# Optimization experiments

Hardware: AMD Instinct MI355X
Metric: run time of the kernel (lower is better)

## Reference

```python
import jax, jax.numpy as jnp
import numpy as np

EPS = 1e-5
INF = 1e5


def setup_inputs() -> dict:
    key = jax.random.key(0)
    ks = iter(jax.random.split(key, 32))
    B, N, F, H, NH, C = 2, 384, 64, 64, 4, 32
    def lin(k, fi, fo):
        return jax.random.normal(k, (fi, fo), jnp.float32) / np.sqrt(fi).astype(np.float32)
    d = {}
    d['h'] = jax.random.normal(next(ks), (B, N, F), jnp.float32)
    d['x'] = jax.random.normal(next(ks), (B, N, 3), jnp.float32)
    # edge_model (ConcatenationFilter): Linear(2F+1,H), SiLU, Linear(H,H), SiLU
    d['We0'] = lin(next(ks), 2 * F + 1, H); d['be0'] = jnp.zeros(H, jnp.float32)
    d['We1'] = lin(next(ks), H, H);         d['be1'] = jnp.zeros(H, jnp.float32)
    # semantic_attention_mlp: Linear(H, n_heads), LeakyReLU(0.2)
    d['Ws'] = lin(next(ks), H, NH);         d['bs'] = jnp.zeros(NH, jnp.float32)
    # coefficients_mlp: Linear(H,H), SiLU, Linear(H,C)
    d['Wc0'] = lin(next(ks), H, H);         d['bc0'] = jnp.zeros(H, jnp.float32)
    d['Wc1'] = lin(next(ks), H, C);         d['bc1'] = jnp.zeros(C, jnp.float32)
    # post_norm_mlp: Linear(C,H), SiLU, Linear(H,H)
    d['Wp0'] = lin(next(ks), C, H);         d['bp0'] = jnp.zeros(H, jnp.float32)
    d['Wp1'] = lin(next(ks), H, H);         d['bp1'] = jnp.zeros(H, jnp.float32)
    # coordinate_mlp: Linear(H,H), SiLU, Linear(H,1,bias=False) init gain 1e-3
    d['Wx0'] = lin(next(ks), H, H);         d['bx0'] = jnp.zeros(H, jnp.float32)
    d['Wx1'] = lin(next(ks), H, 1) * 1e-3
    # node_mlp: Linear(NH*H + H + F, H), SiLU, Linear(H, F)
    d['Wn0'] = lin(next(ks), NH * H + H + F, H); d['bn0'] = jnp.zeros(H, jnp.float32)
    d['Wn1'] = lin(next(ks), H, F);         d['bn1'] = jnp.zeros(F, jnp.float32)
    d['log_gamma'] = jnp.zeros(NH, jnp.float32)
    return d


def _forward(h, x, We0, be0, We1, be1, Ws, bs, Wc0, bc0, Wc1, bc1,
             Wp0, bp0, Wp1, bp1, Wx0, bx0, Wx1, Wn0, bn0, Wn1, bn1, log_gamma):
    B, N, F = h.shape
    silu = jax.nn.silu

    # pairwise displacements and distances: (B,N,N,3), (B,N,N,1)
    x_minus_xt = x[:, :, None, :] - x[:, None, :, :]
    norm = jnp.sqrt(jnp.sum(x_minus_xt * x_minus_xt, axis=-1, keepdims=True) + EPS)

    # pairwise node-feature concat + distance -> edge MLP (ConcatenationFilter)
    hi = jnp.broadcast_to(h[:, :, None, :], (B, N, N, F))
    hj = jnp.broadcast_to(h[:, None, :, :], (B, N, N, F))
    e_in = jnp.concatenate([hi, hj, norm], axis=-1)           # (B,N,N,2F+1)
    h_e = silu(silu(e_in @ We0 + be0) @ We1 + be1)            # (B,N,N,H)

    eye = jnp.eye(N, dtype=h.dtype)[None, :, :, None]         # mask self-edges

    # euclidean attention per head, softmax over neighbors j (axis=-2)
    eu = jax.nn.softmax(-(norm + INF * eye) * jnp.exp(log_gamma), axis=-2)  # (B,N,N,NH)
    # semantic attention
    sem_logits = jax.nn.leaky_relu(h_e @ Ws + bs, 0.2) - INF * eye
    sem = jax.nn.softmax(sem_logits, axis=-2)                 # (B,N,N,NH)
    comb = eu * sem
    comb = comb / (jnp.sum(comb, axis=-2, keepdims=True) + EPS)

    # attention-weighted multi-head edge features, aggregated over neighbors
    h_e_att = (comb[..., :, None] * h_e[..., None, :]).reshape(B, N, N, -1)  # (B,N,N,NH*H)
    h_e_agg = jnp.sum(h_e_att, axis=-2)                       # (B,N,NH*H)

    # spatial attention: equivariant combinations of unit direction vectors
    coeff = silu(h_e @ Wc0 + bc0) @ Wc1 + bc1                 # (B,N,N,C)
    x_hat = x_minus_xt / (norm + EPS)                         # (B,N,N,3)
    combinations = coeff[..., :, None] * x_hat[..., None, :]  # (B,N,N,C,3)
    comb_sum = jnp.mean(combinations, axis=2)                 # mean over j -> (B,N,C,3)
    comb_norm = jnp.sum(comb_sum * comb_sum, axis=-1)         # (B,N,C)
    h_comb = silu(comb_norm @ Wp0 + bp0) @ Wp1 + bp1          # (B,N,H)

    # node update (residual)
    node_in = jnp.concatenate([h, h_e_agg, h_comb], axis=-1)
    h_out = h + (silu(node_in @ Wn0 + bn0) @ Wn1 + bn1)

    # coordinate update: scalar-gated displacements, mean over neighbors
    scale = silu(h_e @ Wx0 + bx0) @ Wx1                       # (B,N,N,1)
    x_out = x + jnp.mean(x_minus_xt * scale, axis=2)          # (B,N,3)
    return h_out, x_out


def reference(h, x, We0, be0, We1, be1, Ws, bs, Wc0, bc0, Wc1, bc1,
              Wp0, bp0, Wp1, bp1, Wx0, bx0, Wx1, Wn0, bn0, Wn1, bn1, log_gamma):
    return _forward(h, x, We0, be0, We1, be1, Ws, bs, Wc0, bc0, Wc1, bc1,
                    Wp0, bp0, Wp1, bp1, Wx0, bx0, Wx1, Wn0, bn0, Wn1, bn1, log_gamma)
```

## Files before the change

kernel.cpp:

```cpp
#include <hip/hip_runtime.h>

#define NPT 384
#define NB 2
#define NROW (NB*NPT)
#define NT 6
#define HOFF 49152
#define RECB 1024
#define REC_OFF 424960

typedef unsigned short u16;
typedef unsigned int u32;
typedef __bf16 bf16x8 __attribute__((ext_vector_type(8)));
typedef float f32x4 __attribute__((ext_vector_type(4)));

struct alignas(16) U4 { u32 x, y, z, w; };
struct alignas(8)  U2 { u32 x, y; };

constexpr float kEPS = 1e-5f;
constexpr float kINF = 1e5f;

__device__ __forceinline__ u16 f2b(float f) { __bf16 b = (__bf16)f; return __builtin_bit_cast(u16, b); }
__device__ __forceinline__ u32 pk2(float lo, float hi) { return (u32)f2b(lo) | ((u32)f2b(hi) << 16); }
__device__ __forceinline__ float b2f(u32 u) { return __uint_as_float(u << 16); }
__device__ __forceinline__ float silu_f(float v) { return v * __builtin_amdgcn_rcpf(1.f + __expf(-v)); }
__device__ __forceinline__ float wredmax(float v) {
#pragma unroll
  for (int m = 32; m >= 1; m >>= 1) v = fmaxf(v, __shfl_xor(v, m, 64));
  return v;
}
__device__ __forceinline__ float wredsum(float v) {
#pragma unroll
  for (int m = 32; m >= 1; m >>= 1) v += __shfl_xor(v, m, 64);
  return v;
}
__device__ __forceinline__ void up8(U4 u, float* f) {
  f[0] = b2f(u.x & 0xffffu); f[1] = b2f(u.x >> 16);
  f[2] = b2f(u.y & 0xffffu); f[3] = b2f(u.y >> 16);
  f[4] = b2f(u.z & 0xffffu); f[5] = b2f(u.z >> 16);
  f[6] = b2f(u.w & 0xffffu); f[7] = b2f(u.w >> 16);
}

__global__ __launch_bounds__(64) void sake_prep(
    const float* __restrict__ h, const float* __restrict__ We0,
    const float* __restrict__ be0, const float* __restrict__ We1,
    const float* __restrict__ Wc0, const float* __restrict__ Wc1,
    const float* __restrict__ Wx0, const float* __restrict__ Ws,
    float* __restrict__ U, float* __restrict__ V, u16* __restrict__ WT)
{
  const int t = threadIdx.x;
  const int blk = blockIdx.x;
  if (blk < NROW) {
    __shared__ float hs[64];
    hs[t] = h[blk * 64 + t];
    __syncthreads();
    float u = be0[t], v = 0.f;
#pragma unroll 8
    for (int k = 0; k < 64; k++) {
      float hv = hs[k];
      u = fmaf(hv, We0[k * 64 + t], u);
      v = fmaf(hv, We0[(64 + k) * 64 + t], v);
    }
    U[blk * 64 + t] = u;
    V[blk * 64 + t] = v;
  } else {
    const int wsel = blk - NROW;
    if (wsel == 4) {
      u16* dst = WT + 14336;
      for (int o = t; o < 16 * 64; o += 64) {
        int c = o >> 6, k = o & 63;
        dst[o] = (c < 4) ? f2b(Ws[k * 4 + c]) : (u16)0;
      }
      return;
    }
    const float* src; int nout; u16* dst;
    if      (wsel == 0) { src = We1; nout = 64; dst = WT;         }
    else if (wsel == 1) { src = Wc0; nout = 64; dst = WT + 4096;  }
    else if (wsel == 2) { src = Wx0; nout = 64; dst = WT + 8192;  }
    else                { src = Wc1; nout = 32; dst = WT + 12288; }
    const int total = 64 * nout;
    for (int o = t; o < total; o += 64) {
      int n = o >> 6, k = o & 63;
      dst[o] = f2b(src[k * nout + n]);
    }
  }
}

struct MainArgs {
  const float *x, *U, *V;
  const u16 *We1T, *Wc0T, *Wx0T, *Wc1T, *WsPT;
  const float *We0, *bs, *be1, *bc0, *bc1, *bx0, *Wx1, *log_gamma;
  char* rec;
};

__device__ __forceinline__ void readB(const u16* tile, int j, int kg, bf16x8& f0, bf16x8& f1) {
  const int r7 = j & 7;
  f0 = *(const bf16x8*)(tile + j * 64 + ((kg ^ r7) << 3));
  f1 = *(const bf16x8*)(tile + j * 64 + (((kg + 4) ^ r7) << 3));
}

template<int NNT, bool SILU_, int NCH, bool DUALT>
__device__ __forceinline__ void gemmT(const u16* __restrict__ wG, const float* __restrict__ biasG,
                                      bf16x8 bf0, bf16x8 bf1, u16* out, u16* oTT, int w, int lane)
{
  const int j = (w << 4) + (lane & 15);
  const int kg = lane >> 4;
  const int jm = j & (NCH - 1);
#pragma unroll
  for (int nt = 0; nt < NNT; nt++) {
    const int nrow = (nt << 4) + (lane & 15);
    bf16x8 a0 = *(const bf16x8*)(wG + nrow * 64 + (kg << 3));
    bf16x8 a1 = *(const bf16x8*)(wG + nrow * 64 + 32 + (kg << 3));
    f32x4 acc = {0.f, 0.f, 0.f, 0.f};
    acc = __builtin_amdgcn_mfma_f32_16x16x32_bf16(a0, bf0, acc, 0, 0, 0);
    acc = __builtin_amdgcn_mfma_f32_16x16x32_bf16(a1, bf1, acc, 0, 0, 0);
    const int n0 = (nt << 4) + (kg << 2);
    const float4 bv = *(const float4*)(biasG + n0);
    float s0, s1, s2, s3;
    if constexpr (SILU_) {
      s0 = silu_f(acc[0] + bv.x); s1 = silu_f(acc[1] + bv.y);
      s2 = silu_f(acc[2] + bv.z); s3 = silu_f(acc[3] + bv.w);
    } else {
      s0 = acc[0] + bv.x; s1 = acc[1] + bv.y;
      s2 = acc[2] + bv.z; s3 = acc[3] + bv.w;
    }
    const u16 q0 = f2b(s0), q1 = f2b(s1), q2 = f2b(s2), q3 = f2b(s3);
    U2 pkd; pkd.x = (u32)q0 | ((u32)q1 << 16); pkd.y = (u32)q2 | ((u32)q3 << 16);
    const int c = n0 >> 3;
    *(U2*)(out + j * (NCH * 8) + (((c ^ jm) << 3) + (n0 & 7))) = pkd;
    if constexpr (DUALT) {
      const int jq = (j >> 3), j7 = j & 7;
      const u16 qs[4] = {q0, q1, q2, q3};
#pragma unroll
      for (int r = 0; r < 4; r++) {
        const int f = n0 + r;
        oTT[f * 64 + ((jq ^ (f & 7)) << 3) + j7] = qs[r];
      }
    }
  }
}

__global__ __launch_bounds__(256, 4) void sake_main(MainArgs A)
{
  __shared__ __align__(16) u16 buf0[64 * 64];
  __shared__ __align__(16) u16 hes[64 * 64];
  __shared__ __align__(16) u16 hesT[64 * 64];
  __shared__ __align__(16) u16 coeff[64 * 32];
  __shared__ __align__(16) u16 E_lds[16 * 64];
  __shared__ float raw_lds[64 * 5];
  __shared__ float disp[64][3];
  __shared__ float nrm_s[64];

  const int t = threadIdx.x;
  const int w = t >> 6, lane = t & 63;
  const int bt = blockIdx.x;
  const int i = bt % NPT;
  const int bj = bt / NPT;
  const int jt = bj % NT, b = bj / NT;
  const int bi = b * NPT + i;
  const int j0 = jt << 6;
  const int jj2 = t >> 2, q4 = t & 3;
  char* rec = A.rec + (size_t)(bi * NT + jt) * RECB;

  const int jrow = j0 + jj2;
  const float* xp = &A.x[(b * NPT + jrow) * 3];
  const float xj0 = xp[0], xj1 = xp[1], xj2 = xp[2];
  const float xi0 = A.x[bi * 3 + 0], xi1 = A.x[bi * 3 + 1], xi2 = A.x[bi * 3 + 2];
  const float4* vp = (const float4*)(A.V + (size_t)(b * NPT + jrow) * 64 + q4 * 16);
  const float4 v0_ = vp[0], v1_ = vp[1], v2_ = vp[2], v3_ = vp[3];
  const float4* Up = (const float4*)(A.U + bi * 64 + q4 * 16);
  const float4 u0_ = Up[0], u1_ = Up[1], u2_ = Up[2], u3_ = Up[3];
  const float4* Wd = (const float4*)(A.We0 + 128 * 64 + q4 * 16);
  const float4 w0_ = Wd[0], w1_ = Wd[1], w2_ = Wd[2], w3_ = Wd[3];

  {
    float dx0 = xi0 - xj0, dx1 = xi1 - xj1, dx2 = xi2 - xj2;
    float nr = sqrtf(fmaf(dx0, dx0, fmaf(dx1, dx1, fmaf(dx2, dx2, kEPS))));
    if (q4 == 0) { disp[jj2][0] = dx0; disp[jj2][1] = dx1; disp[jj2][2] = dx2; nrm_s[jj2] = nr; }
    float vv[16] = {v0_.x, v0_.y, v0_.z, v0_.w, v1_.x, v1_.y, v1_.z, v1_.w,
                    v2_.x, v2_.y, v2_.z, v2_.w, v3_.x, v3_.y, v3_.z, v3_.w};
    float uu[16] = {u0_.x, u0_.y, u0_.z, u0_.w, u1_.x, u1_.y, u1_.z, u1_.w,
                    u2_.x, u2_.y, u2_.z, u2_.w, u3_.x, u3_.y, u3_.z, u3_.w};
    float ww[16] = {w0_.x, w0_.y, w0_.z, w0_.w, w1_.x, w1_.y, w1_.z, w1_.w,
                    w2_.x, w2_.y, w2_.z, w2_.w, w3_.x, w3_.y, w3_.z, w3_.w};
    float sv[16];
#pragma unroll
    for (int e = 0; e < 16; e++) sv[e] = silu_f(uu[e] + vv[e] + nr * ww[e]);
    U4 lo, hi;
    lo.x = pk2(sv[0], sv[1]);   lo.y = pk2(sv[2], sv[3]);
    lo.z = pk2(sv[4], sv[5]);   lo.w = pk2(sv[6], sv[7]);
    hi.x = pk2(sv[8], sv[9]);   hi.y = pk2(sv[10], sv[11]);
    hi.z = pk2(sv[12], sv[13]); hi.w = pk2(sv[14], sv[15]);
    const int r7 = jj2 & 7;
    *(U4*)(buf0 + jj2 * 64 + (((q4 * 2) ^ r7) << 3)) = lo;
    *(U4*)(buf0 + jj2 * 64 + (((q4 * 2 + 1) ^ r7) << 3)) = hi;
  }

  const int j = (w << 4) + (lane & 15);
  const int kg = lane >> 4;

  bf16x8 bh0, bh1;
  readB(buf0, j, kg, bh0, bh1);
  gemmT<4, true, 8, true>(A.We1T, A.be1, bh0, bh1, hes, hesT, w, lane);

  bf16x8 he0, he1;
  readB(hes, j, kg, he0, he1);

  gemmT<4, true, 8, false>(A.Wc0T, A.bc0, he0, he1, buf0, nullptr, w, lane);
  bf16x8 c10, c11;
  readB(buf0, j, kg, c10, c11);
  gemmT<2, false, 4, false>(A.Wc1T, A.bc1, c10, c11, coeff, nullptr, w, lane);

  float cA0 = 0, cA1 = 0, cA2 = 0, xA0 = 0, xA1 = 0, xA2 = 0;
  {
    const int c = t & 31, g = t >> 5;
    const int cc = c >> 3, ce = c & 7;
#pragma unroll
    for (int it = 0; it < 8; ++it) {
      const int jj = (g << 3) + it;
      const float s = b2f(coeff[jj * 32 + ((cc ^ (jj & 3)) << 3) + ce]) *
                      __builtin_amdgcn_rcpf(nrm_s[jj] + kEPS);
      cA0 = fmaf(s, disp[jj][0], cA0);
      cA1 = fmaf(s, disp[jj][1], cA1);
      cA2 = fmaf(s, disp[jj][2], cA2);
    }
  }

  gemmT<4, true, 8, false>(A.Wx0T, A.bx0, he0, he1, buf0, nullptr, w, lane);

  {
    const int jj = jj2;
    const int r7 = jj & 7;
    float acc = 0.f;
#pragma unroll
    for (int c2 = 0; c2 < 2; c2++) {
      const int c = q4 * 2 + c2;
      U4 u = *(const U4*)(buf0 + jj * 64 + ((c ^ r7) << 3));
      float f8[8]; up8(u, f8);
      const float4* wx = (const float4*)(A.Wx1 + c * 8);
      const float4 wxa = wx[0], wxb = wx[1];
      acc = fmaf(f8[0], wxa.x, acc); acc = fmaf(f8[1], wxa.y, acc);
      acc = fmaf(f8[2], wxa.z, acc); acc = fmaf(f8[3], wxa.w, acc);
      acc = fmaf(f8[4], wxb.x, acc); acc = fmaf(f8[5], wxb.y, acc);
      acc = fmaf(f8[6], wxb.z, acc); acc = fmaf(f8[7], wxb.w, acc);
    }
    acc += __shfl_xor(acc, 1, 64);
    acc += __shfl_xor(acc, 2, 64);
    if (q4 == 0) {
      xA0 = fmaf(disp[jj][0], acc, xA0);
      xA1 = fmaf(disp[jj][1], acc, xA1);
      xA2 = fmaf(disp[jj][2], acc, xA2);
    }
  }

  {
    const int m0 = w << 4;
    const int arow = m0 + (lane & 15);
    const int r7a = arow & 7;
    bf16x8 a0 = *(const bf16x8*)(hes + arow * 64 + ((kg ^ r7a) << 3));
    bf16x8 a1 = *(const bf16x8*)(hes + arow * 64 + (((kg + 4) ^ r7a) << 3));
    const u16* wrow = A.WsPT + (lane & 15) * 64;
    bf16x8 b0 = *(const bf16x8*)(wrow + (kg << 3));
    bf16x8 b1 = *(const bf16x8*)(wrow + 32 + (kg << 3));
    f32x4 acc = {0.f, 0.f, 0.f, 0.f};
    acc = __builtin_amdgcn_mfma_f32_16x16x32_bf16(a0, b0, acc, 0, 0, 0);
    acc = __builtin_amdgcn_mfma_f32_16x16x32_bf16(a1, b1, acc, 0, 0, 0);
    if ((lane & 15) < 4) {
#pragma unroll
      for (int r = 0; r < 4; r++)
        raw_lds[(m0 + (kg << 2) + r) * 5 + (lane & 15)] = acc[r];
    }
  }
  __syncthreads();

  float* cascr = (float*)buf0;
  float* xscr = (float*)buf0 + 768;
  cascr[t * 3 + 0] = cA0; cascr[t * 3 + 1] = cA1; cascr[t * 3 + 2] = cA2;
  if (q4 == 0) { xscr[jj2 * 3 + 0] = xA0; xscr[jj2 * 3 + 1] = xA1; xscr[jj2 * 3 + 2] = xA2; }

  {
    const int jj = lane, head = w;
    float raw = raw_lds[jj * 5 + head] + A.bs[head];
    float bsem = (raw > 0.f) ? raw : 0.2f * raw;
    const bool self = (j0 + jj) == i;
    if (self) bsem -= kINF;
    const float gam = __expf(A.log_gamma[head]);
    const float aeu = -(nrm_s[jj] + (self ? kINF : 0.f)) * gam;
    const float L = aeu + bsem;
    const float mL = wredmax(L);
    const float eL = __expf(L - mL);
    const float SL = wredsum(eL);
    const float mb = wredmax(bsem);
    const float Sb = wredsum(__expf(bsem - mb));
    const float Sa = wredsum(__expf(aeu));
    E_lds[head * 64 + (((jj >> 3) ^ head) << 3) + (jj & 7)] = f2b(eL);
    if (lane == 0) {
      float* sp = (float*)(rec + 908) + head * 5;
      sp[0] = mL; sp[1] = SL; sp[2] = mb; sp[3] = Sb; sp[4] = Sa;
    }
  }
  __syncthreads();

  {
    const int erow = lane & 15;
    const int e7 = erow & 7;
    bf16x8 ea0 = *(const bf16x8*)(E_lds + erow * 64 + ((kg ^ e7) << 3));
    bf16x8 ea1 = *(const bf16x8*)(E_lds + erow * 64 + (((kg + 4) ^ e7) << 3));
    const int f = (w << 4) + (lane & 15);
    const int f7 = f & 7;
    bf16x8 hb0 = *(const bf16x8*)(hesT + f * 64 + ((kg ^ f7) << 3));
    bf16x8 hb1 = *(const bf16x8*)(hesT + f * 64 + (((kg + 4) ^ f7) << 3));
    f32x4 aF = {0.f, 0.f, 0.f, 0.f};
    aF = __builtin_amdgcn_mfma_f32_16x16x32_bf16(ea0, hb0, aF, 0, 0, 0);
    aF = __builtin_amdgcn_mfma_f32_16x16x32_bf16(ea1, hb1, aF, 0, 0, 0);
    if (kg == 0) {
      u16* rA = (u16*)rec;
#pragma unroll
      for (int r = 0; r < 4; r++) rA[r * 64 + f] = f2b(aF[r]);
    }
  }
  if (t < 96) {
    const int c = t & 31, d = t >> 5;
    float s = 0.f;
#pragma unroll
    for (int g = 0; g < 8; g++) s += cascr[(g * 32 + c) * 3 + d];
    ((float*)(rec + 512))[d * 32 + c] = s;
  } else if (t < 99) {
    const int d = t - 96;
    float s = 0.f;
    for (int k = 0; k < 64; k++) s += xscr[k * 3 + d];
    ((float*)(rec + 896))[d] = s;
  }
}

struct MergeArgs {
  const float *h, *x, *Wp0, *bp0, *Wp1, *bp1, *Wn0, *bn0, *Wn1, *bn1;
  const char* rec;
  float* out;
};

__global__ __launch_bounds__(256) void sake_merge(MergeArgs M)
{
  __shared__ float sc[NT][20];
  __shared__ float wAl[NT][4];
  __shared__ float coefh[4];
  __shared__ float node_in[384];
  __shared__ float cmv[96];
  __shared__ float nrm32[32];
  __shared__ float t0s[64];
  __shared__ float scr[256];

  const int t = threadIdx.x;
  const int bi = blockIdx.x;
  const char* rb = M.rec + (size_t)bi * NT * RECB;

  if (t < NT * 20) {
    const int tt = t / 20, k = t % 20;
    sc[tt][k] = ((const float*)(rb + tt * RECB + 908))[k];
  }
  if (t < 64) node_in[t] = M.h[bi * 64 + t];
  __syncthreads();
  if (t < 4) {
    const int hh = t;
    float mL = -1e30f, mb = -1e30f;
    for (int tt = 0; tt < NT; tt++) {
      mL = fmaxf(mL, sc[tt][hh * 5 + 0]);
      mb = fmaxf(mb, sc[tt][hh * 5 + 2]);
    }
    float SL = 0.f, Sb = 0.f, Sa = 0.f;
    for (int tt = 0; tt < NT; tt++) {
      const float wa = __expf(sc[tt][hh * 5 + 0] - mL);
      wAl[tt][hh] = wa;
      SL = fmaf(wa, sc[tt][hh * 5 + 1], SL);
      Sb = fmaf(__expf(sc[tt][hh * 5 + 2] - mb), sc[tt][hh * 5 + 3], Sb);
      Sa += sc[tt][hh * 5 + 4];
    }
    const float Ff = __expf(mL - mb);
    coefh[hh] = Ff / fmaf(SL, Ff, kEPS * Sa * Sb);
  }
  __syncthreads();
  {
    const int hh = t >> 6, f = t & 63;
    float s = 0.f;
#pragma unroll
    for (int tt = 0; tt < NT; tt++)
      s = fmaf(wAl[tt][hh], b2f(((const u16*)(rb + tt * RECB))[hh * 64 + f]), s);
    node_in[64 + hh * 64 + f] = s * coefh[hh];
  }
  if (t < 96) {
    float s = 0.f;
#pragma unroll
    for (int tt = 0; tt < NT; tt++) s += ((const float*)(rb + tt * RECB + 512))[t];
    cmv[t] = s * (1.f / 384.f);
  }
  if (t >= 128 && t < 131) {
    const int d = t - 128;
    float s = 0.f;
#pragma unroll
    for (int tt = 0; tt < NT; tt++) s += ((const float*)(rb + tt * RECB + 896))[d];
    M.out[HOFF + bi * 3 + d] = M.x[bi * 3 + d] + s * (1.f / 384.f);
  }
  __syncthreads();
  if (t < 32) {
    const float v0 = cmv[t], v1 = cmv[32 + t], v2 = cmv[64 + t];
    nrm32[t] = v0 * v0 + v1 * v1 + v2 * v2;
  }
  __syncthreads();
  if (t < 64) {
    float a = M.bp0[t];
    for (int c = 0; c < 32; c++) a = fmaf(nrm32[c], M.Wp0[c * 64 + t], a);
    t0s[t] = silu_f(a);
  }
  __syncthreads();
  if (t < 64) {
    float a = M.bp1[t];
    for (int k = 0; k < 64; k++) a = fmaf(t0s[k], M.Wp1[k * 64 + t], a);
    node_in[320 + t] = a;
  }
  __syncthreads();
  {
    const int f = t & 63, q = t >> 6;
    float a = 0.f;
    const int k0 = q * 96;
    for (int k = 0; k < 96; k++) a = fmaf(node_in[k0 + k], M.Wn0[(k0 + k) * 64 + f], a);
    scr[t] = a;
  }
  __syncthreads();
  if (t < 64) {
    const float s = scr[t] + scr[64 + t] + scr[128 + t] + scr[192 + t] + M.bn0[t];
    t0s[t] = silu_f(s);
  }
  __syncthreads();
  if (t < 64) {
    float a = M.bn1[t];
    for (int k = 0; k < 64; k++) a = fmaf(t0s[k], M.Wn1[k * 64 + t], a);
    M.out[bi * 64 + t] = M.h[bi * 64 + t] + a;
  }
}

extern "C" void kernel_launch(void* const* d_in, const int* in_sizes, int n_in,
                              void* d_out, int out_size, void* d_ws, size_t ws_size,
                              hipStream_t stream)
{
  (void)in_sizes; (void)n_in; (void)out_size; (void)ws_size;
  const float* h   = (const float*)d_in[0];
  const float* x   = (const float*)d_in[1];
  const float* We0 = (const float*)d_in[2];
  const float* be0 = (const float*)d_in[3];
  const float* We1 = (const float*)d_in[4];
  const float* be1 = (const float*)d_in[5];
  const float* Ws  = (const float*)d_in[6];
  const float* bs  = (const float*)d_in[7];
  const float* Wc0 = (const float*)d_in[8];
  const float* bc0 = (const float*)d_in[9];
  const float* Wc1 = (const float*)d_in[10];
  const float* bc1 = (const float*)d_in[11];
  const float* Wp0 = (const float*)d_in[12];
  const float* bp0 = (const float*)d_in[13];
  const float* Wp1 = (const float*)d_in[14];
  const float* bp1 = (const float*)d_in[15];
  const float* Wx0 = (const float*)d_in[16];
  const float* bx0 = (const float*)d_in[17];
  const float* Wx1 = (const float*)d_in[18];
  const float* Wn0 = (const float*)d_in[19];
  const float* bn0 = (const float*)d_in[20];
  const float* Wn1 = (const float*)d_in[21];
  const float* bn1 = (const float*)d_in[22];
  const float* lg  = (const float*)d_in[23];

  float* U = (float*)d_ws;
  float* V = U + NROW * 64;
  u16* WT = (u16*)(V + NROW * 64);
  char* rec = (char*)d_ws + REC_OFF;

  sake_prep<<<NROW + 5, 64, 0, stream>>>(h, We0, be0, We1, Wc0, Wc1, Wx0, Ws, U, V, WT);

  MainArgs A;
  A.x = x; A.U = U; A.V = V;
  A.We1T = WT; A.Wc0T = WT + 4096; A.Wx0T = WT + 8192; A.Wc1T = WT + 12288;
  A.WsPT = WT + 14336;
  A.We0 = We0; A.bs = bs; A.be1 = be1; A.bc0 = bc0; A.bc1 = bc1;
  A.bx0 = bx0; A.Wx1 = Wx1; A.log_gamma = lg;
  A.rec = rec;
  sake_main<<<NROW * NT, 256, 0, stream>>>(A);

  MergeArgs Mg;
  Mg.h = h; Mg.x = x;
  Mg.Wp0 = Wp0; Mg.bp0 = bp0; Mg.Wp1 = Wp1; Mg.bp1 = bp1;
  Mg.Wn0 = Wn0; Mg.bn0 = bn0; Mg.Wn1 = Wn1; Mg.bn1 = bn1;
  Mg.rec = rec; Mg.out = (float*)d_out;
  sake_merge<<<NROW, 256, 0, stream>>>(Mg);
}
```

Measured before the change: 104.3 us.

## Double block size to 512 threads, split GEMM output columns across wave pairs

The main kernel now runs with 512 threads per block. Each pair of waves shares a 16-row strip, and each wave computes half of every GEMM's output columns. The attention-softmax work runs on four waves while the coordinate-gate reduction runs concurrently on the other four. More waves per block give more latency hiding and overlap, in exchange for extra __syncthreads barriers, a doubled partial-sum reduction, and higher register and occupancy pressure under launch_bounds(512, 8).

```diff
diff --git a/kernel.cpp b/kernel.cpp
--- a/kernel.cpp
+++ b/kernel.cpp
@@ -14,7 +14,6 @@
 typedef float f32x4 __attribute__((ext_vector_type(4)));
 
 struct alignas(16) U4 { u32 x, y, z, w; };
-struct alignas(8)  U2 { u32 x, y; };
 
 constexpr float kEPS = 1e-5f;
 constexpr float kINF = 1e5f;
@@ -99,21 +98,20 @@
 }
 
 template<int NNT, bool SILU_, int NCH, bool DUALT>
-__device__ __forceinline__ void gemmT(const u16* __restrict__ wG, const float* __restrict__ biasG,
-                                      bf16x8 bf0, bf16x8 bf1, u16* out, u16* oTT, int w, int lane)
+__device__ __forceinline__ void gemmT8(const u16* __restrict__ wG, const float* __restrict__ biasG,
+                                       bf16x8 bf0, bf16x8 bf1, u16* out, u16* oTT,
+                                       int j, int kg, int l15, int nbase)
 {
-  const int j = (w << 4) + (lane & 15);
-  const int kg = lane >> 4;
   const int jm = j & (NCH - 1);
 #pragma unroll
   for (int nt = 0; nt < NNT; nt++) {
-    const int nrow = (nt << 4) + (lane & 15);
+    const int nrow = nbase + (nt << 4) + l15;
     bf16x8 a0 = *(const bf16x8*)(wG + nrow * 64 + (kg << 3));
     bf16x8 a1 = *(const bf16x8*)(wG + nrow * 64 + 32 + (kg << 3));
     f32x4 acc = {0.f, 0.f, 0.f, 0.f};
     acc = __builtin_amdgcn_mfma_f32_16x16x32_bf16(a0, bf0, acc, 0, 0, 0);
     acc = __builtin_amdgcn_mfma_f32_16x16x32_bf16(a1, bf1, acc, 0, 0, 0);
-    const int n0 = (nt << 4) + (kg << 2);
+    const int n0 = nbase + (nt << 4) + (kg << 2);
     const float4 bv = *(const float4*)(biasG + n0);
     float s0, s1, s2, s3;
     if constexpr (SILU_) {
@@ -124,9 +122,10 @@
       s2 = acc[2] + bv.z; s3 = acc[3] + bv.w;
     }
     const u16 q0 = f2b(s0), q1 = f2b(s1), q2 = f2b(s2), q3 = f2b(s3);
-    U2 pkd; pkd.x = (u32)q0 | ((u32)q1 << 16); pkd.y = (u32)q2 | ((u32)q3 << 16);
+    u32 pkx = (u32)q0 | ((u32)q1 << 16), pky = (u32)q2 | ((u32)q3 << 16);
     const int c = n0 >> 3;
-    *(U2*)(out + j * (NCH * 8) + (((c ^ jm) << 3) + (n0 & 7))) = pkd;
+    u32* dst = (u32*)(out + j * (NCH * 8) + (((c ^ jm) << 3) + (n0 & 7)));
+    dst[0] = pkx; dst[1] = pky;
     if constexpr (DUALT) {
       const int jq = (j >> 3), j7 = j & 7;
       const u16 qs[4] = {q0, q1, q2, q3};
@@ -139,7 +138,7 @@
   }
 }
 
-__global__ __launch_bounds__(256, 4) void sake_main(MainArgs A)
+__global__ __launch_bounds__(512, 8) void sake_main(MainArgs A)
 {
   __shared__ __align__(16) u16 buf0[64 * 64];
   __shared__ __align__(16) u16 hes[64 * 64];
@@ -152,71 +151,92 @@
 
   const int t = threadIdx.x;
   const int w = t >> 6, lane = t & 63;
+  const int rs = w >> 1, ch = w & 1;
+  const int kg = lane >> 4, l15 = lane & 15;
   const int bt = blockIdx.x;
   const int i = bt % NPT;
   const int bj = bt / NPT;
   const int jt = bj % NT, b = bj / NT;
   const int bi = b * NPT + i;
   const int j0 = jt << 6;
-  const int jj2 = t >> 2, q4 = t & 3;
   char* rec = A.rec + (size_t)(bi * NT + jt) * RECB;
 
-  const int jrow = j0 + jj2;
-  const float* xp = &A.x[(b * NPT + jrow) * 3];
-  const float xj0 = xp[0], xj1 = xp[1], xj2 = xp[2];
-  const float xi0 = A.x[bi * 3 + 0], xi1 = A.x[bi * 3 + 1], xi2 = A.x[bi * 3 + 2];
-  const float4* vp = (const float4*)(A.V + (size_t)(b * NPT + jrow) * 64 + q4 * 16);
-  const float4 v0_ = vp[0], v1_ = vp[1], v2_ = vp[2], v3_ = vp[3];
-  const float4* Up = (const float4*)(A.U + bi * 64 + q4 * 16);
-  const float4 u0_ = Up[0], u1_ = Up[1], u2_ = Up[2], u3_ = Up[3];
-  const float4* Wd = (const float4*)(A.We0 + 128 * 64 + q4 * 16);
-  const float4 w0_ = Wd[0], w1_ = Wd[1], w2_ = Wd[2], w3_ = Wd[3];
-
-  {
+  const int jj3 = t >> 3, q8 = t & 7;
+  {
+    const int jrow = j0 + jj3;
+    const float* xp = &A.x[(b * NPT + jrow) * 3];
+    const float xj0 = xp[0], xj1 = xp[1], xj2 = xp[2];
+    const float xi0 = A.x[bi * 3 + 0], xi1 = A.x[bi * 3 + 1], xi2 = A.x[bi * 3 + 2];
+    const float4* vp = (const float4*)(A.V + (size_t)(b * NPT + jrow) * 64 + q8 * 8);
+    const float4 v0_ = vp[0], v1_ = vp[1];
+    const float4* Up = (const float4*)(A.U + bi * 64 + q8 * 8);
+    const float4 u0_ = Up[0], u1_ = Up[1];
+    const float4* Wd = (const float4*)(A.We0 + 128 * 64 + q8 * 8);
+    const float4 w0_ = Wd[0], w1_ = Wd[1];
     float dx0 = xi0 - xj0, dx1 = xi1 - xj1, dx2 = xi2 - xj2;
     float nr = sqrtf(fmaf(dx0, dx0, fmaf(dx1, dx1, fmaf(dx2, dx2, kEPS))));
-    if (q4 == 0) { disp[jj2][0] = dx0; disp[jj2][1] = dx1; disp[jj2][2] = dx2; nrm_s[jj2] = nr; }
-    float vv[16] = {v0_.x, v0_.y, v0_.z, v0_.w, v1_.x, v1_.y, v1_.z, v1_.w,
-                    v2_.x, v2_.y, v2_.z, v2_.w, v3_.x, v3_.y, v3_.z, v3_.w};
-    float uu[16] = {u0_.x, u0_.y, u0_.z, u0_.w, u1_.x, u1_.y, u1_.z, u1_.w,
-                    u2_.x, u2_.y, u2_.z, u2_.w, u3_.x, u3_.y, u3_.z, u3_.w};
-    float ww[16] = {w0_.x, w0_.y, w0_.z, w0_.w, w1_.x, w1_.y, w1_.z, w1_.w,
-                    w2_.x, w2_.y, w2_.z, w2_.w, w3_.x, w3_.y, w3_.z, w3_.w};
-    float sv[16];
-#pragma unroll
-    for (int e = 0; e < 16; e++) sv[e] = silu_f(uu[e] + vv[e] + nr * ww[e]);
-    U4 lo, hi;
-    lo.x = pk2(sv[0], sv[1]);   lo.y = pk2(sv[2], sv[3]);
-    lo.z = pk2(sv[4], sv[5]);   lo.w = pk2(sv[6], sv[7]);
-    hi.x = pk2(sv[8], sv[9]);   hi.y = pk2(sv[10], sv[11]);
-    hi.z = pk2(sv[12], sv[13]); hi.w = pk2(sv[14], sv[15]);
-    const int r7 = jj2 & 7;
-    *(U4*)(buf0 + jj2 * 64 + (((q4 * 2) ^ r7) << 3)) = lo;
-    *(U4*)(buf0 + jj2 * 64 + (((q4 * 2 + 1) ^ r7) << 3)) = hi;
-  }
-
-  const int j = (w << 4) + (lane & 15);
-  const int kg = lane >> 4;
-
-  bf16x8 bh0, bh1;
-  readB(buf0, j, kg, bh0, bh1);
-  gemmT<4, true, 8, true>(A.We1T, A.be1, bh0, bh1, hes, hesT, w, lane);
+    if (q8 == 0) { disp[jj3][0] = dx0; disp[jj3][1] = dx1; disp[jj3][2] = dx2; nrm_s[jj3] = nr; }
+    float vv[8] = {v0_.x, v0_.y, v0_.z, v0_.w, v1_.x, v1_.y, v1_.z, v1_.w};
+    float uu[8] = {u0_.x, u0_.y, u0_.z, u0_.w, u1_.x, u1_.y, u1_.z, u1_.w};
+    float ww[8] = {w0_.x, w0_.y, w0_.z, w0_.w, w1_.x, w1_.y, w1_.z, w1_.w};
+    float sv[8];
+#pragma unroll
+    for (int e = 0; e < 8; e++) sv[e] = silu_f(uu[e] + vv[e] + nr * ww[e]);
+    U4 u4;
+    u4.x = pk2(sv[0], sv[1]); u4.y = pk2(sv[2], sv[3]);
+    u4.z = pk2(sv[4], sv[5]); u4.w = pk2(sv[6], sv[7]);
+    *(U4*)(buf0 + jj3 * 64 + ((q8 ^ (jj3 & 7)) << 3)) = u4;
+  }
+  __syncthreads();
+
+  const int jrow16 = (rs << 4) + l15;
+  const int nb64 = ch << 5;
+
+  {
+    bf16x8 bh0, bh1;
+    readB(buf0, jrow16, kg, bh0, bh1);
+    gemmT8<2, true, 8, true>(A.We1T, A.be1, bh0, bh1, hes, hesT, jrow16, kg, l15, nb64);
+  }
+  __syncthreads();
 
   bf16x8 he0, he1;
-  readB(hes, j, kg, he0, he1);
-
-  gemmT<4, true, 8, false>(A.Wc0T, A.bc0, he0, he1, buf0, nullptr, w, lane);
-  bf16x8 c10, c11;
-  readB(buf0, j, kg, c10, c11);
-  gemmT<2, false, 4, false>(A.Wc1T, A.bc1, c10, c11, coeff, nullptr, w, lane);
+  readB(hes, jrow16, kg, he0, he1);
+
+  gemmT8<2, true, 8, false>(A.Wc0T, A.bc0, he0, he1, buf0, nullptr, jrow16, kg, l15, nb64);
+  __syncthreads();
+
+  {
+    bf16x8 c10, c11;
+    readB(buf0, jrow16, kg, c10, c11);
+    gemmT8<1, false, 4, false>(A.Wc1T, A.bc1, c10, c11, coeff, nullptr, jrow16, kg, l15, ch << 4);
+  }
+  if (ch == 0) {
+    const int m0 = rs << 4;
+    const int arow = m0 + l15;
+    const int r7a = arow & 7;
+    bf16x8 a0 = *(const bf16x8*)(hes + arow * 64 + ((kg ^ r7a) << 3));
+    bf16x8 a1 = *(const bf16x8*)(hes + arow * 64 + (((kg + 4) ^ r7a) << 3));
+    const u16* wrow = A.WsPT + l15 * 64;
+    bf16x8 b0 = *(const bf16x8*)(wrow + (kg << 3));
+    bf16x8 b1 = *(const bf16x8*)(wrow + 32 + (kg << 3));
+    f32x4 acc = {0.f, 0.f, 0.f, 0.f};
+    acc = __builtin_amdgcn_mfma_f32_16x16x32_bf16(a0, b0, acc, 0, 0, 0);
+    acc = __builtin_amdgcn_mfma_f32_16x16x32_bf16(a1, b1, acc, 0, 0, 0);
+    if (l15 < 4) {
+#pragma unroll
+      for (int r = 0; r < 4; r++)
+        raw_lds[(m0 + (kg << 2) + r) * 5 + l15] = acc[r];
+    }
+  }
+  __syncthreads();
 
   float cA0 = 0, cA1 = 0, cA2 = 0, xA0 = 0, xA1 = 0, xA2 = 0;
   {
     const int c = t & 31, g = t >> 5;
     const int cc = c >> 3, ce = c & 7;
 #pragma unroll
-    for (int it = 0; it < 8; ++it) {
-      const int jj = (g << 3) + it;
+    for (int it = 0; it < 4; ++it) {
+      const int jj = (g << 2) + it;
       const float s = b2f(coeff[jj * 32 + ((cc ^ (jj & 3)) << 3) + ce]) *
                       __builtin_amdgcn_rcpf(nrm_s[jj] + kEPS);
       cA0 = fmaf(s, disp[jj][0], cA0);
@@ -224,60 +244,11 @@
       cA2 = fmaf(s, disp[jj][2], cA2);
     }
   }
-
-  gemmT<4, true, 8, false>(A.Wx0T, A.bx0, he0, he1, buf0, nullptr, w, lane);
-
-  {
-    const int jj = jj2;
-    const int r7 = jj & 7;
-    float acc = 0.f;
-#pragma unroll
-    for (int c2 = 0; c2 < 2; c2++) {
-      const int c = q4 * 2 + c2;
-      U4 u = *(const U4*)(buf0 + jj * 64 + ((c ^ r7) << 3));
-      float f8[8]; up8(u, f8);
-      const float4* wx = (const float4*)(A.Wx1 + c * 8);
-      const float4 wxa = wx[0], wxb = wx[1];
-      acc = fmaf(f8[0], wxa.x, acc); acc = fmaf(f8[1], wxa.y, acc);
-      acc = fmaf(f8[2], wxa.z, acc); acc = fmaf(f8[3], wxa.w, acc);
-      acc = fmaf(f8[4], wxb.x, acc); acc = fmaf(f8[5], wxb.y, acc);
-      acc = fmaf(f8[6], wxb.z, acc); acc = fmaf(f8[7], wxb.w, acc);
-    }
-    acc += __shfl_xor(acc, 1, 64);
-    acc += __shfl_xor(acc, 2, 64);
-    if (q4 == 0) {
-      xA0 = fmaf(disp[jj][0], acc, xA0);
-      xA1 = fmaf(disp[jj][1], acc, xA1);
-      xA2 = fmaf(disp[jj][2], acc, xA2);
-    }
-  }
-
-  {
-    const int m0 = w << 4;
-    const int arow = m0 + (lane & 15);
-    const int r7a = arow & 7;
-    bf16x8 a0 = *(const bf16x8*)(hes + arow * 64 + ((kg ^ r7a) << 3));
-    bf16x8 a1 = *(const bf16x8*)(hes + arow * 64 + (((kg + 4) ^ r7a) << 3));
-    const u16* wrow = A.WsPT + (lane & 15) * 64;
-    bf16x8 b0 = *(const bf16x8*)(wrow + (kg << 3));
-    bf16x8 b1 = *(const bf16x8*)(wrow + 32 + (kg << 3));
-    f32x4 acc = {0.f, 0.f, 0.f, 0.f};
-    acc = __builtin_amdgcn_mfma_f32_16x16x32_bf16(a0, b0, acc, 0, 0, 0);
-    acc = __builtin_amdgcn_mfma_f32_16x16x32_bf16(a1, b1, acc, 0, 0, 0);
-    if ((lane & 15) < 4) {
-#pragma unroll
-      for (int r = 0; r < 4; r++)
-        raw_lds[(m0 + (kg << 2) + r) * 5 + (lane & 15)] = acc[r];
-    }
-  }
-  __syncthreads();
-
-  float* cascr = (float*)buf0;
-  float* xscr = (float*)buf0 + 768;
-  cascr[t * 3 + 0] = cA0; cascr[t * 3 + 1] = cA1; cascr[t * 3 + 2] = cA2;
-  if (q4 == 0) { xscr[jj2 * 3 + 0] = xA0; xscr[jj2 * 3 + 1] = xA1; xscr[jj2 * 3 + 2] = xA2; }
-
-  {
+  gemmT8<2, true, 8, false>(A.Wx0T, A.bx0, he0, he1, buf0, nullptr, jrow16, kg, l15, nb64);
+  __syncthreads();
+
+  float mL_r = 0.f, SL_r = 0.f, mb_r = 0.f, Sb_r = 0.f, Sa_r = 0.f;
+  if (w < 4) {
     const int jj = lane, head = w;
     float raw = raw_lds[jj * 5 + head] + A.bs[head];
     float bsem = (raw > 0.f) ? raw : 0.2f * raw;
@@ -293,19 +264,51 @@
     const float Sb = wredsum(__expf(bsem - mb));
     const float Sa = wredsum(__expf(aeu));
     E_lds[head * 64 + (((jj >> 3) ^ head) << 3) + (jj & 7)] = f2b(eL);
-    if (lane == 0) {
-      float* sp = (float*)(rec + 908) + head * 5;
-      sp[0] = mL; sp[1] = SL; sp[2] = mb; sp[3] = Sb; sp[4] = Sa;
-    }
-  }
-  __syncthreads();
-
-  {
-    const int erow = lane & 15;
+    mL_r = mL; SL_r = SL; mb_r = mb; Sb_r = Sb; Sa_r = Sa;
+  } else {
+    const int tp = t - 256;
+    const int jj = tp >> 2, q4 = tp & 3;
+    const int r7 = jj & 7;
+    float acc = 0.f;
+#pragma unroll
+    for (int c2 = 0; c2 < 2; c2++) {
+      const int c = q4 * 2 + c2;
+      U4 u = *(const U4*)(buf0 + jj * 64 + ((c ^ r7) << 3));
+      float f8[8]; up8(u, f8);
+      const float4* wx = (const float4*)(A.Wx1 + c * 8);
+      const float4 wxa = wx[0], wxb = wx[1];
+      acc = fmaf(f8[0], wxa.x, acc); acc = fmaf(f8[1], wxa.y, acc);
+      acc = fmaf(f8[2], wxa.z, acc); acc = fmaf(f8[3], wxa.w, acc);
+      acc = fmaf(f8[4], wxb.x, acc); acc = fmaf(f8[5], wxb.y, acc);
+      acc = fmaf(f8[6], wxb.z, acc); acc = fmaf(f8[7], wxb.w, acc);
+    }
+    acc += __shfl_xor(acc, 1, 64);
+    acc += __shfl_xor(acc, 2, 64);
+    if (q4 == 0) {
+      xA0 = disp[jj][0] * acc;
+      xA1 = disp[jj][1] * acc;
+      xA2 = disp[jj][2] * acc;
+    }
+  }
+  if (w < 4 && lane == 0) {
+    float* sp = (float*)(rec + 908) + w * 5;
+    sp[0] = mL_r; sp[1] = SL_r; sp[2] = mb_r; sp[3] = Sb_r; sp[4] = Sa_r;
+  }
+  __syncthreads();
+
+  float* cascr = (float*)buf0;
+  float* xscr = (float*)hes;
+  cascr[t * 3 + 0] = cA0; cascr[t * 3 + 1] = cA1; cascr[t * 3 + 2] = cA2;
+  if (w >= 4 && ((t - 256) & 3) == 0) {
+    const int jj = (t - 256) >> 2;
+    xscr[jj * 3 + 0] = xA0; xscr[jj * 3 + 1] = xA1; xscr[jj * 3 + 2] = xA2;
+  }
+  if (w < 4) {
+    const int erow = l15;
     const int e7 = erow & 7;
     bf16x8 ea0 = *(const bf16x8*)(E_lds + erow * 64 + ((kg ^ e7) << 3));
     bf16x8 ea1 = *(const bf16x8*)(E_lds + erow * 64 + (((kg + 4) ^ e7) << 3));
-    const int f = (w << 4) + (lane & 15);
+    const int f = (w << 4) + l15;
     const int f7 = f & 7;
     bf16x8 hb0 = *(const bf16x8*)(hesT + f * 64 + ((kg ^ f7) << 3));
     bf16x8 hb1 = *(const bf16x8*)(hesT + f * 64 + (((kg + 4) ^ f7) << 3));
@@ -318,11 +321,13 @@
       for (int r = 0; r < 4; r++) rA[r * 64 + f] = f2b(aF[r]);
     }
   }
+  __syncthreads();
+
   if (t < 96) {
     const int c = t & 31, d = t >> 5;
     float s = 0.f;
 #pragma unroll
-    for (int g = 0; g < 8; g++) s += cascr[(g * 32 + c) * 3 + d];
+    for (int g = 0; g < 16; g++) s += cascr[(g * 32 + c) * 3 + d];
     ((float*)(rec + 512))[d * 32 + c] = s;
   } else if (t < 99) {
     const int d = t - 96;
@@ -481,7 +486,7 @@
   A.We0 = We0; A.bs = bs; A.be1 = be1; A.bc0 = bc0; A.bc1 = bc1;
   A.bx0 = bx0; A.Wx1 = Wx1; A.log_gamma = lg;
   A.rec = rec;
-  sake_main<<<NROW * NT, 256, 0, stream>>>(A);
+  sake_main<<<NROW * NT, 512, 0, stream>>>(A);
 
   MergeArgs Mg;
   Mg.h = h; Mg.x = x;
```

Result: faster. 99.94 us (-4.2%).
